# Performance work log

Measured on AMD Instinct MI355X. Metric: run time of the kernel, lower is better.

The kernel has to match this reference:

```python
import jax, jax.numpy as jnp
from jax import lax
import numpy as np

EPS = 1e-08
BETA_VAL = 0.9
B_VAL = 1.0
SIGMA_VAL = 10.0

@jax.custom_vjp
def spike_fn(mthr, sigma):
    # Heaviside forward; SuperSpike surrogate gradient in backward
    return (mthr > 0).astype(mthr.dtype)

def _spike_fwd(mthr, sigma):
    return (mthr > 0).astype(mthr.dtype), (mthr, sigma)

def _spike_bwd(res, g):
    mthr, sigma = res
    grad = g / (sigma * jnp.abs(mthr) + 1.0) ** 2
    return grad, jnp.zeros_like(sigma)

spike_fn.defvjp(_spike_fwd, _spike_bwd)


def setup_inputs() -> dict:
    key = jax.random.key(0)
    kx, kw, kv = jax.random.split(key, 3)
    B, T, I, O = 128, 100, 1024, 1024
    x = jax.random.normal(kx, (B, T, I), dtype=jnp.float32)
    w = (jax.random.normal(kw, (I, O), dtype=jnp.float32)
         * np.float32(np.sqrt(1.0 / I)))  # mean 0, std w_init_std*sqrt(1/I)
    v = (jax.random.normal(kv, (O, O), dtype=jnp.float32)
         * np.float32(np.sqrt(1.0 / O)))
    beta = jnp.full((1,), BETA_VAL, dtype=jnp.float32)   # one_per_layer
    b = jnp.full((O,), B_VAL, dtype=jnp.float32)
    sigma = jnp.full((O,), SIGMA_VAL, dtype=jnp.float32)  # surrogate_sigma_mode='all'
    return {"x": x, "w": w, "v": v, "beta": beta, "b": b, "sigma": sigma}


def reference(x, w, v, beta, b, sigma):
    B, T, I = x.shape
    O = w.shape[1]
    h = jnp.einsum('bti,io->bto', x, w)            # [B,T,O]
    d = jnp.einsum('ai,ao->io', w, w)              # lateral term w^T w, [O,O]
    norm = (w ** 2).sum(0)                         # [O]
    inv_norm = 1.0 / (norm + EPS)

    mem0 = jnp.zeros((B, O), dtype=x.dtype)
    spk0 = jnp.zeros((B, O), dtype=x.dtype)

    def step(carry, h_t):
        mem, spk = carry
        rst = spk @ d                              # lateral reset [B,O]
        inp = h_t + spk @ v                        # recurrent input
        # Leaky neuron, soft reset
        mem = (mem - rst) * beta + inp * (1.0 - beta)
        mthr = mem * inv_norm - b
        spk = spike_fn(mthr, sigma)
        return (mem, spk), spk

    h_t_first = jnp.swapaxes(h, 0, 1)              # [T,B,O]
    _, spk_seq = lax.scan(step, (mem0, spk0), h_t_first)
    spk_rec = jnp.swapaxes(spk_seq, 0, 1)          # [B,T,O]

    loss = 0.5 * (spk_rec ** 2).mean()             # Regularization 'squared'
    spk_spread_loss = spk_rec.sum(axis=(0, 2)).max() / (B * O)  # 'max'
    return spk_rec, loss, spk_spread_loss
```

## Files before the change

### kernel.cpp

```cpp
#include <hip/hip_runtime.h>
#include <cstdint>
#include <cstddef>

#define I_DIM 1024
#define O_DIM 1024
#define B_DIM 128
#define T_DIM 100
#define PANEL 32768
#define QSTep 512

typedef __attribute__((ext_vector_type(8))) __bf16 bf16x8;
typedef __attribute__((ext_vector_type(16))) float f32x16;

__device__ __forceinline__ void wg_barrier_lgkm() {
  __asm__ volatile("" ::: "memory");
  __builtin_amdgcn_s_waitcnt(0xC07F);
  __builtin_amdgcn_s_barrier();
  __asm__ volatile("" ::: "memory");
}

__device__ __forceinline__ unsigned short bf16rn(float x) {
  unsigned u = __float_as_uint(x);
  unsigned r = u + 0x7FFFu + ((u >> 16) & 1u);
  return (unsigned short)(r >> 16);
}
__device__ __forceinline__ void split2(float x, unsigned short& h,
                                       unsigned short& l) {
  h = bf16rn(x);
  float hf = __uint_as_float(((unsigned)h) << 16);
  l = bf16rn(x - hf);
}

__global__ __launch_bounds__(256) void prep_kernel(
    const float* __restrict__ w, const float* __restrict__ x,
    unsigned short* __restrict__ wTth, unsigned short* __restrict__ wTtl,
    unsigned short* __restrict__ xth, unsigned short* __restrict__ xtl,
    double* __restrict__ normpart) {
  __shared__ float tile[64][65];
  __shared__ double red[4][64];
  const int id = blockIdx.x;
  const int tid = threadIdx.x;
  if (id < 256) {
    const int a0 = (id >> 4) * 64, o0 = (id & 15) * 64;
    const int tr = tid >> 4, tc4 = (tid & 15) * 4;
#pragma unroll
    for (int rr = 0; rr < 64; rr += 16) {
      float4 v = *(const float4*)&w[(size_t)(a0 + tr + rr) * O_DIM + o0 + tc4];
      tile[tr + rr][tc4 + 0] = v.x;
      tile[tr + rr][tc4 + 1] = v.y;
      tile[tr + rr][tc4 + 2] = v.z;
      tile[tr + rr][tc4 + 3] = v.w;
    }
    __syncthreads();
    {
      const int ol = tid & 63, seg = tid >> 6;
      double s = 0.0;
#pragma unroll
      for (int i = 0; i < 16; ++i) {
        double v = (double)tile[seg * 16 + i][ol];
        s += v * v;
      }
      red[seg][ol] = s;
    }
    const int q = (a0 >> 4) + (tc4 >> 4);
    const int kh = (tc4 >> 3) & 1;
    const int inner = tc4 & 7;
#pragma unroll
    for (int rr = 0; rr < 64; rr += 16) {
      int o = o0 + tr + rr;
      unsigned short hh[4], ll[4];
#pragma unroll
      for (int j = 0; j < 4; ++j) split2(tile[tc4 + j][tr + rr], hh[j], ll[j]);
      int l = (o & 31) + 32 * kh;
      size_t base = ((size_t)(o >> 5) * PANEL) + (size_t)q * QSTep +
                    (size_t)l * 8 + inner;
      *(ushort4*)&wTth[base] = make_ushort4(hh[0], hh[1], hh[2], hh[3]);
      *(ushort4*)&wTtl[base] = make_ushort4(ll[0], ll[1], ll[2], ll[3]);
    }
    __syncthreads();
    if (tid < 64)
      normpart[(size_t)(a0 >> 6) * O_DIM + o0 + tid] =
          red[0][tid] + red[1][tid] + red[2][tid] + red[3][tid];
  } else {
    const int p = id - 256;
    const int wq = tid >> 6, lane = tid & 63;
    const int row = lane & 31, kh = lane >> 5;
    const float* src = x + (size_t)(p * 32 + row) * I_DIM + kh * 8;
#pragma unroll 4
    for (int i = 0; i < 16; ++i) {
      const int q = i * 4 + wq;
      const float* s = src + q * 16;
      float4 v0 = *(const float4*)(s);
      float4 v1 = *(const float4*)(s + 4);
      unsigned short h[8], l[8];
      split2(v0.x, h[0], l[0]);
      split2(v0.y, h[1], l[1]);
      split2(v0.z, h[2], l[2]);
      split2(v0.w, h[3], l[3]);
      split2(v1.x, h[4], l[4]);
      split2(v1.y, h[5], l[5]);
      split2(v1.z, h[6], l[6]);
      split2(v1.w, h[7], l[7]);
      size_t base = ((size_t)p * PANEL) + (size_t)q * QSTep + (size_t)lane * 8;
      *(ushort4*)&xth[base] = make_ushort4(h[0], h[1], h[2], h[3]);
      *(ushort4*)&xth[base + 4] = make_ushort4(h[4], h[5], h[6], h[7]);
      *(ushort4*)&xtl[base] = make_ushort4(l[0], l[1], l[2], l[3]);
      *(ushort4*)&xtl[base + 4] = make_ushort4(l[4], l[5], l[6], l[7]);
    }
  }
}

__global__ __launch_bounds__(256) void gemm_fused(
    const unsigned short* __restrict__ xth,
    const unsigned short* __restrict__ xtl,
    const unsigned short* __restrict__ wTth,
    const unsigned short* __restrict__ wTtl, const float* __restrict__ v,
    const float* __restrict__ beta_p, float* __restrict__ h,
    float* __restrict__ M) {
  const int tid = threadIdx.x;
  const int wv = tid >> 6, lane = tid & 63;
  const int lm = lane & 31, lkh = lane >> 5;
  if (blockIdx.y < 100) {
    const int row0 = blockIdx.y * 128, col0 = blockIdx.x * 64;
    const int wm = wv >> 1, wn = wv & 1;
    f32x16 acc[2];
#pragma unroll
    for (int a = 0; a < 2; ++a)
#pragma unroll
      for (int e = 0; e < 16; ++e) acc[a][e] = 0.f;
    const unsigned short *pah[2], *pal[2], *pbh, *pbl;
#pragma unroll
    for (int mt = 0; mt < 2; ++mt) {
      size_t offA =
          ((size_t)((row0 >> 5) + wm * 2 + mt) * PANEL) + (size_t)lane * 8;
      pah[mt] = xth + offA;
      pal[mt] = xtl + offA;
    }
    {
      size_t offB = ((size_t)((col0 >> 5) + wn) * PANEL) + (size_t)lane * 8;
      pbh = wTth + offB;
      pbl = wTtl + offB;
    }
    bf16x8 fah[2][2], fal[2][2], fbh[2], fbl[2];
#pragma unroll
    for (int mt = 0; mt < 2; ++mt) {
      fah[0][mt] = *(const bf16x8*)(pah[mt]);
      fal[0][mt] = *(const bf16x8*)(pal[mt]);
    }
    fbh[0] = *(const bf16x8*)(pbh);
    fbl[0] = *(const bf16x8*)(pbl);
#pragma unroll 2
    for (int q = 0; q < 64; ++q) {
      const int cb = q & 1;
      if (q < 63) {
        size_t d = (size_t)(q + 1) * QSTep;
#pragma unroll
        for (int mt = 0; mt < 2; ++mt) {
          fah[cb ^ 1][mt] = *(const bf16x8*)(pah[mt] + d);
          fal[cb ^ 1][mt] = *(const bf16x8*)(pal[mt] + d);
        }
        fbh[cb ^ 1] = *(const bf16x8*)(pbh + d);
        fbl[cb ^ 1] = *(const bf16x8*)(pbl + d);
      }
#pragma unroll
      for (int mt = 0; mt < 2; ++mt)
        acc[mt] = __builtin_amdgcn_mfma_f32_32x32x16_bf16(fah[cb][mt], fbh[cb],
                                                          acc[mt], 0, 0, 0);
#pragma unroll
      for (int mt = 0; mt < 2; ++mt)
        acc[mt] = __builtin_amdgcn_mfma_f32_32x32x16_bf16(fah[cb][mt], fbl[cb],
                                                          acc[mt], 0, 0, 0);
#pragma unroll
      for (int mt = 0; mt < 2; ++mt)
        acc[mt] = __builtin_amdgcn_mfma_f32_32x32x16_bf16(fal[cb][mt], fbh[cb],
                                                          acc[mt], 0, 0, 0);
    }
    const int col = col0 + wn * 32 + lm;
#pragma unroll
    for (int mt = 0; mt < 2; ++mt)
#pragma unroll
      for (int r = 0; r < 16; ++r) {
        int row = row0 + wm * 64 + mt * 32 + (r & 3) + 8 * (r >> 2) + 4 * lkh;
        h[(size_t)row * O_DIM + col] = acc[mt][r];
      }
  } else {
    const int i0 = (blockIdx.y - 100) * 64, o0 = blockIdx.x * 64;
    const int wm = wv >> 1, wn = wv & 1;
    f32x16 acc;
#pragma unroll
    for (int e = 0; e < 16; ++e) acc[e] = 0.f;
    const size_t offA = ((size_t)((i0 >> 5) + wm) * PANEL) + (size_t)lane * 8;
    const size_t offB = ((size_t)((o0 >> 5) + wn) * PANEL) + (size_t)lane * 8;
    bf16x8 ah[2], al[2], bh[2], bl[2];
    ah[0] = *(const bf16x8*)(wTth + offA);
    al[0] = *(const bf16x8*)(wTtl + offA);
    bh[0] = *(const bf16x8*)(wTth + offB);
    bl[0] = *(const bf16x8*)(wTtl + offB);
#pragma unroll 2
    for (int q = 0; q < 64; ++q) {
      const int cb = q & 1;
      if (q < 63) {
        size_t d = (size_t)(q + 1) * QSTep;
        ah[cb ^ 1] = *(const bf16x8*)(wTth + offA + d);
        al[cb ^ 1] = *(const bf16x8*)(wTtl + offA + d);
        bh[cb ^ 1] = *(const bf16x8*)(wTth + offB + d);
        bl[cb ^ 1] = *(const bf16x8*)(wTtl + offB + d);
      }
      acc =
          __builtin_amdgcn_mfma_f32_32x32x16_bf16(ah[cb], bh[cb], acc, 0, 0, 0);
      acc =
          __builtin_amdgcn_mfma_f32_32x32x16_bf16(ah[cb], bl[cb], acc, 0, 0, 0);
      acc =
          __builtin_amdgcn_mfma_f32_32x32x16_bf16(al[cb], bh[cb], acc, 0, 0, 0);
    }
    const float beta = beta_p[0];
    const float ombeta = 1.0f - beta;
    const int col = o0 + wn * 32 + lm;
#pragma unroll
    for (int r = 0; r < 16; ++r) {
      int row = i0 + wm * 32 + (r & 3) + 8 * (r >> 2) + 4 * lkh;
      M[(size_t)row * O_DIM + col] =
          ombeta * v[(size_t)row * O_DIM + col] - beta * acc[r];
    }
  }
}

__global__ __launch_bounds__(256) void scan_kernel(
    const float* __restrict__ h, const float* __restrict__ M,
    const double* __restrict__ normpart, const float* __restrict__ bvec,
    const float* __restrict__ beta_p, float* __restrict__ out,
    int* __restrict__ wgcnt) {
  __shared__ unsigned short wlist[2][4][256];
  __shared__ int wcnt[2][4];
  const int b = blockIdx.x, tid = threadIdx.x;
  const int wv = tid >> 6;
  const double beta = (double)beta_p[0];
  const double ombeta = 1.0 - beta;
  double mem[4] = {0.0, 0.0, 0.0, 0.0};
  double inv[4], bth[4];
  int o[4];
#pragma unroll
  for (int j = 0; j < 4; ++j) {
    o[j] = tid + j * 256;
    double s = 0.0;
#pragma unroll
    for (int g = 0; g < 16; ++g) s += normpart[(size_t)g * O_DIM + o[j]];
    inv[j] = 1.0 / (s + 1e-8);
    bth[j] = (double)bvec[o[j]];
  }
  if (tid < 8) wcnt[tid >> 2][tid & 3] = 0;
  __syncthreads();
  const float* hb = h + (size_t)b * T_DIM * O_DIM;
  float* ob = out + (size_t)b * T_DIM * O_DIM;
  float hv0[4], hv1[4];
#pragma unroll
  for (int j = 0; j < 4; ++j) {
    hv0[j] = hb[o[j]];
    hv1[j] = hb[O_DIM + o[j]];
  }
  for (int t = 0; t < T_DIM; ++t) {
    const int p = t & 1, np = p ^ 1;
    float hv2[4] = {0.f, 0.f, 0.f, 0.f};
    if (t + 2 < T_DIM) {
#pragma unroll
      for (int j = 0; j < 4; ++j) hv2[j] = hb[(size_t)(t + 2) * O_DIM + o[j]];
    }
    double lat[4] = {0.0, 0.0, 0.0, 0.0};
    const int ks = wcnt[p][0] + wcnt[p][1] + wcnt[p][2] + wcnt[p][3];
    if (ks) {
#pragma unroll
      for (int w = 0; w < 4; ++w) {
        const int kw = wcnt[p][w];
        for (int n = 0; n < kw; ++n) {
          const int i = wlist[p][w][n];
          const float* Mrow = M + (size_t)i * O_DIM;
#pragma unroll
          for (int j = 0; j < 4; ++j) lat[j] += (double)Mrow[o[j]];
        }
      }
    }
    unsigned cur = 0;
#pragma unroll
    for (int j = 0; j < 4; ++j) {
      mem[j] = mem[j] * beta + (double)hv0[j] * ombeta + lat[j];
      double mthr = mem[j] * inv[j] - bth[j];
      bool s = mthr > 0.0;
      ob[(size_t)t * O_DIM + o[j]] = s ? 1.0f : 0.0f;
      unsigned long long mask = __ballot(s);
      if (s) {
        unsigned below = __builtin_amdgcn_mbcnt_lo((unsigned)mask, 0);
        below = __builtin_amdgcn_mbcnt_hi((unsigned)(mask >> 32), below);
        wlist[np][wv][cur + below] = (unsigned short)o[j];
      }
      cur += (unsigned)__popcll(mask);
      hv0[j] = hv1[j];
      hv1[j] = hv2[j];
    }
    if ((tid & 63) == 0) wcnt[np][wv] = (int)cur;
    wg_barrier_lgkm();
    if (tid == 0)
      wgcnt[b * T_DIM + t] =
          wcnt[np][0] + wcnt[np][1] + wcnt[np][2] + wcnt[np][3];
  }
}

__global__ void finalize_kernel(const int* __restrict__ wgcnt,
                                float* __restrict__ out) {
  __shared__ int sums[128];
  const int t = threadIdx.x;
  int s = 0;
  if (t < T_DIM) {
    for (int b = 0; b < B_DIM; ++b) s += wgcnt[b * T_DIM + t];
  }
  sums[t] = s;
  __syncthreads();
  if (t == 0) {
    long long total = 0;
    int mx = 0;
    for (int i = 0; i < T_DIM; ++i) {
      total += sums[i];
      if (sums[i] > mx) mx = sums[i];
    }
    const double N = (double)B_DIM * T_DIM * O_DIM;
    out[(size_t)B_DIM * T_DIM * O_DIM] = (float)(0.5 * (double)total / N);
    out[(size_t)B_DIM * T_DIM * O_DIM + 1] =
        (float)((double)mx / (double)(B_DIM * O_DIM));
  }
}

extern "C" void kernel_launch(void* const* d_in, const int* in_sizes, int n_in,
                              void* d_out, int out_size, void* d_ws,
                              size_t ws_size, hipStream_t stream) {
  const float* x = (const float*)d_in[0];
  const float* w = (const float*)d_in[1];
  const float* v = (const float*)d_in[2];
  const float* beta = (const float*)d_in[3];
  const float* b = (const float*)d_in[4];
  float* out = (float*)d_out;

  char* ws = (char*)d_ws;
  const size_t OFF_M = 0;
  const size_t OFF_H = 4194304;
  const size_t OFF_WTH = 56623104;
  const size_t OFF_WTL = 58720256;
  const size_t OFF_NP = 60817408;
  const size_t OFF_XTH = 60948992;
  const size_t OFF_XTL = 87163392;
  float* M = (float*)(ws + OFF_M);
  float* h = (float*)(ws + OFF_H);
  unsigned short* wTth = (unsigned short*)(ws + OFF_WTH);
  unsigned short* wTtl = (unsigned short*)(ws + OFF_WTL);
  double* normpart = (double*)(ws + OFF_NP);
  unsigned short* xth = (unsigned short*)(ws + OFF_XTH);
  unsigned short* xtl = (unsigned short*)(ws + OFF_XTL);
  int* wgcnt = (int*)(ws + OFF_XTH);

  hipLaunchKernelGGL(prep_kernel, dim3(656), dim3(256), 0, stream, w, x, wTth,
                     wTtl, xth, xtl, normpart);
  hipLaunchKernelGGL(gemm_fused, dim3(16, 116), dim3(256), 0, stream, xth, xtl,
                     wTth, wTtl, v, beta, h, M);
  hipLaunchKernelGGL(scan_kernel, dim3(128), dim3(256), 0, stream, h, M,
                     normpart, b, beta, out, wgcnt);
  hipLaunchKernelGGL(finalize_kernel, dim3(1), dim3(128), 0, stream, wgcnt,
                     out);
}
```

Baseline: 306.5 us.

## Split x prep across more blocks, deepen GEMM prefetch, vectorize scan, fuse finalize

Splits each x panel conversion into four blocks so prep launches 1856 blocks instead of 656, giving more parallelism. The GEMM now prefetches two K-steps per iteration and sets launch bounds to three blocks per CU. The scan kernel gives each thread four contiguous outputs so it can use float4 loads of h and M and float4 stores of spikes. The separate finalize kernel is removed: the last scan block to finish, found through an atomic counter, computes the two losses, which saves one launch but adds a memset and a fence.

```diff
diff --git a/kernel.cpp b/kernel.cpp
--- a/kernel.cpp
+++ b/kernel.cpp
@@ -82,12 +82,12 @@
       normpart[(size_t)(a0 >> 6) * O_DIM + o0 + tid] =
           red[0][tid] + red[1][tid] + red[2][tid] + red[3][tid];
   } else {
-    const int p = id - 256;
+    const int p = (id - 256) >> 2, sub = (id - 256) & 3;
     const int wq = tid >> 6, lane = tid & 63;
     const int row = lane & 31, kh = lane >> 5;
     const float* src = x + (size_t)(p * 32 + row) * I_DIM + kh * 8;
-#pragma unroll 4
-    for (int i = 0; i < 16; ++i) {
+#pragma unroll
+    for (int i = sub * 4; i < sub * 4 + 4; ++i) {
       const int q = i * 4 + wq;
       const float* s = src + q * 16;
       float4 v0 = *(const float4*)(s);
@@ -110,7 +110,7 @@
   }
 }
 
-__global__ __launch_bounds__(256) void gemm_fused(
+__global__ __launch_bounds__(256, 3) void gemm_fused(
     const unsigned short* __restrict__ xth,
     const unsigned short* __restrict__ xtl,
     const unsigned short* __restrict__ wTth,
@@ -141,39 +141,50 @@
       pbh = wTth + offB;
       pbl = wTtl + offB;
     }
-    bf16x8 fah[2][2], fal[2][2], fbh[2], fbl[2];
-#pragma unroll
-    for (int mt = 0; mt < 2; ++mt) {
-      fah[0][mt] = *(const bf16x8*)(pah[mt]);
-      fal[0][mt] = *(const bf16x8*)(pal[mt]);
-    }
-    fbh[0] = *(const bf16x8*)(pbh);
-    fbl[0] = *(const bf16x8*)(pbl);
+    bf16x8 fah[2][2][2], fal[2][2][2], fbh[2][2], fbl[2][2];
+#pragma unroll
+    for (int qq = 0; qq < 2; ++qq) {
+      size_t d = (size_t)qq * QSTep;
+#pragma unroll
+      for (int mt = 0; mt < 2; ++mt) {
+        fah[0][qq][mt] = *(const bf16x8*)(pah[mt] + d);
+        fal[0][qq][mt] = *(const bf16x8*)(pal[mt] + d);
+      }
+      fbh[0][qq] = *(const bf16x8*)(pbh + d);
+      fbl[0][qq] = *(const bf16x8*)(pbl + d);
+    }
 #pragma unroll 2
-    for (int q = 0; q < 64; ++q) {
-      const int cb = q & 1;
-      if (q < 63) {
-        size_t d = (size_t)(q + 1) * QSTep;
-#pragma unroll
-        for (int mt = 0; mt < 2; ++mt) {
-          fah[cb ^ 1][mt] = *(const bf16x8*)(pah[mt] + d);
-          fal[cb ^ 1][mt] = *(const bf16x8*)(pal[mt] + d);
+    for (int qp = 0; qp < 32; ++qp) {
+      const int cb = qp & 1;
+      if (qp < 31) {
+        size_t dp = (size_t)(qp + 1) * (2 * QSTep);
+#pragma unroll
+        for (int qq = 0; qq < 2; ++qq) {
+          size_t d = dp + (size_t)qq * QSTep;
+#pragma unroll
+          for (int mt = 0; mt < 2; ++mt) {
+            fah[cb ^ 1][qq][mt] = *(const bf16x8*)(pah[mt] + d);
+            fal[cb ^ 1][qq][mt] = *(const bf16x8*)(pal[mt] + d);
+          }
+          fbh[cb ^ 1][qq] = *(const bf16x8*)(pbh + d);
+          fbl[cb ^ 1][qq] = *(const bf16x8*)(pbl + d);
         }
-        fbh[cb ^ 1] = *(const bf16x8*)(pbh + d);
-        fbl[cb ^ 1] = *(const bf16x8*)(pbl + d);
-      }
-#pragma unroll
-      for (int mt = 0; mt < 2; ++mt)
-        acc[mt] = __builtin_amdgcn_mfma_f32_32x32x16_bf16(fah[cb][mt], fbh[cb],
-                                                          acc[mt], 0, 0, 0);
-#pragma unroll
-      for (int mt = 0; mt < 2; ++mt)
-        acc[mt] = __builtin_amdgcn_mfma_f32_32x32x16_bf16(fah[cb][mt], fbl[cb],
-                                                          acc[mt], 0, 0, 0);
-#pragma unroll
-      for (int mt = 0; mt < 2; ++mt)
-        acc[mt] = __builtin_amdgcn_mfma_f32_32x32x16_bf16(fal[cb][mt], fbh[cb],
-                                                          acc[mt], 0, 0, 0);
+      }
+#pragma unroll
+      for (int qq = 0; qq < 2; ++qq) {
+#pragma unroll
+        for (int mt = 0; mt < 2; ++mt)
+          acc[mt] = __builtin_amdgcn_mfma_f32_32x32x16_bf16(
+              fah[cb][qq][mt], fbh[cb][qq], acc[mt], 0, 0, 0);
+#pragma unroll
+        for (int mt = 0; mt < 2; ++mt)
+          acc[mt] = __builtin_amdgcn_mfma_f32_32x32x16_bf16(
+              fah[cb][qq][mt], fbl[cb][qq], acc[mt], 0, 0, 0);
+#pragma unroll
+        for (int mt = 0; mt < 2; ++mt)
+          acc[mt] = __builtin_amdgcn_mfma_f32_32x32x16_bf16(
+              fal[cb][qq][mt], fbh[cb][qq], acc[mt], 0, 0, 0);
+      }
     }
     const int col = col0 + wn * 32 + lm;
 #pragma unroll
@@ -229,42 +240,36 @@
     const float* __restrict__ h, const float* __restrict__ M,
     const double* __restrict__ normpart, const float* __restrict__ bvec,
     const float* __restrict__ beta_p, float* __restrict__ out,
-    int* __restrict__ wgcnt) {
+    int* __restrict__ wgcnt, int* __restrict__ done) {
   __shared__ unsigned short wlist[2][4][256];
   __shared__ int wcnt[2][4];
+  __shared__ int reds[128];
+  __shared__ int lastflag;
   const int b = blockIdx.x, tid = threadIdx.x;
   const int wv = tid >> 6;
+  const int ob4 = tid * 4;
   const double beta = (double)beta_p[0];
   const double ombeta = 1.0 - beta;
   double mem[4] = {0.0, 0.0, 0.0, 0.0};
   double inv[4], bth[4];
-  int o[4];
 #pragma unroll
   for (int j = 0; j < 4; ++j) {
-    o[j] = tid + j * 256;
     double s = 0.0;
 #pragma unroll
-    for (int g = 0; g < 16; ++g) s += normpart[(size_t)g * O_DIM + o[j]];
+    for (int g = 0; g < 16; ++g) s += normpart[(size_t)g * O_DIM + ob4 + j];
     inv[j] = 1.0 / (s + 1e-8);
-    bth[j] = (double)bvec[o[j]];
+    bth[j] = (double)bvec[ob4 + j];
   }
   if (tid < 8) wcnt[tid >> 2][tid & 3] = 0;
   __syncthreads();
   const float* hb = h + (size_t)b * T_DIM * O_DIM;
-  float* ob = out + (size_t)b * T_DIM * O_DIM;
-  float hv0[4], hv1[4];
-#pragma unroll
-  for (int j = 0; j < 4; ++j) {
-    hv0[j] = hb[o[j]];
-    hv1[j] = hb[O_DIM + o[j]];
-  }
+  float* obp = out + (size_t)b * T_DIM * O_DIM;
+  float4 hv0 = *(const float4*)&hb[ob4];
+  float4 hv1 = *(const float4*)&hb[O_DIM + ob4];
   for (int t = 0; t < T_DIM; ++t) {
     const int p = t & 1, np = p ^ 1;
-    float hv2[4] = {0.f, 0.f, 0.f, 0.f};
-    if (t + 2 < T_DIM) {
-#pragma unroll
-      for (int j = 0; j < 4; ++j) hv2[j] = hb[(size_t)(t + 2) * O_DIM + o[j]];
-    }
+    float4 hv2 = make_float4(0.f, 0.f, 0.f, 0.f);
+    if (t + 2 < T_DIM) hv2 = *(const float4*)&hb[(size_t)(t + 2) * O_DIM + ob4];
     double lat[4] = {0.0, 0.0, 0.0, 0.0};
     const int ks = wcnt[p][0] + wcnt[p][1] + wcnt[p][2] + wcnt[p][3];
     if (ks) {
@@ -273,58 +278,67 @@
         const int kw = wcnt[p][w];
         for (int n = 0; n < kw; ++n) {
           const int i = wlist[p][w][n];
-          const float* Mrow = M + (size_t)i * O_DIM;
-#pragma unroll
-          for (int j = 0; j < 4; ++j) lat[j] += (double)Mrow[o[j]];
+          float4 m = *(const float4*)&M[(size_t)i * O_DIM + ob4];
+          lat[0] += (double)m.x;
+          lat[1] += (double)m.y;
+          lat[2] += (double)m.z;
+          lat[3] += (double)m.w;
         }
       }
     }
+    const float hvv[4] = {hv0.x, hv0.y, hv0.z, hv0.w};
+    float os[4];
     unsigned cur = 0;
 #pragma unroll
     for (int j = 0; j < 4; ++j) {
-      mem[j] = mem[j] * beta + (double)hv0[j] * ombeta + lat[j];
+      mem[j] = mem[j] * beta + (double)hvv[j] * ombeta + lat[j];
       double mthr = mem[j] * inv[j] - bth[j];
       bool s = mthr > 0.0;
-      ob[(size_t)t * O_DIM + o[j]] = s ? 1.0f : 0.0f;
+      os[j] = s ? 1.0f : 0.0f;
       unsigned long long mask = __ballot(s);
       if (s) {
         unsigned below = __builtin_amdgcn_mbcnt_lo((unsigned)mask, 0);
         below = __builtin_amdgcn_mbcnt_hi((unsigned)(mask >> 32), below);
-        wlist[np][wv][cur + below] = (unsigned short)o[j];
+        wlist[np][wv][cur + below] = (unsigned short)(ob4 + j);
       }
       cur += (unsigned)__popcll(mask);
-      hv0[j] = hv1[j];
-      hv1[j] = hv2[j];
-    }
+    }
+    *(float4*)&obp[(size_t)t * O_DIM + ob4] =
+        make_float4(os[0], os[1], os[2], os[3]);
+    hv0 = hv1;
+    hv1 = hv2;
     if ((tid & 63) == 0) wcnt[np][wv] = (int)cur;
     wg_barrier_lgkm();
     if (tid == 0)
       wgcnt[b * T_DIM + t] =
           wcnt[np][0] + wcnt[np][1] + wcnt[np][2] + wcnt[np][3];
   }
-}
-
-__global__ void finalize_kernel(const int* __restrict__ wgcnt,
-                                float* __restrict__ out) {
-  __shared__ int sums[128];
-  const int t = threadIdx.x;
-  int s = 0;
-  if (t < T_DIM) {
-    for (int b = 0; b < B_DIM; ++b) s += wgcnt[b * T_DIM + t];
-  }
-  sums[t] = s;
+  __threadfence();
+  if (tid == 0) {
+    int old = atomicAdd(done, 1);
+    lastflag = (old == B_DIM - 1) ? 1 : 0;
+  }
   __syncthreads();
-  if (t == 0) {
-    long long total = 0;
-    int mx = 0;
-    for (int i = 0; i < T_DIM; ++i) {
-      total += sums[i];
-      if (sums[i] > mx) mx = sums[i];
-    }
-    const double N = (double)B_DIM * T_DIM * O_DIM;
-    out[(size_t)B_DIM * T_DIM * O_DIM] = (float)(0.5 * (double)total / N);
-    out[(size_t)B_DIM * T_DIM * O_DIM + 1] =
-        (float)((double)mx / (double)(B_DIM * O_DIM));
+  if (lastflag) {
+    __threadfence();
+    int s = 0;
+    if (tid < T_DIM) {
+      for (int bb = 0; bb < B_DIM; ++bb) s += wgcnt[bb * T_DIM + tid];
+    }
+    if (tid < 128) reds[tid] = (tid < T_DIM) ? s : 0;
+    __syncthreads();
+    if (tid == 0) {
+      long long total = 0;
+      int mx = 0;
+      for (int i = 0; i < T_DIM; ++i) {
+        total += reds[i];
+        if (reds[i] > mx) mx = reds[i];
+      }
+      const double N = (double)B_DIM * T_DIM * O_DIM;
+      out[(size_t)B_DIM * T_DIM * O_DIM] = (float)(0.5 * (double)total / N);
+      out[(size_t)B_DIM * T_DIM * O_DIM + 1] =
+          (float)((double)mx / (double)(B_DIM * O_DIM));
+    }
   }
 }
 
@@ -344,6 +358,7 @@
   const size_t OFF_WTH = 56623104;
   const size_t OFF_WTL = 58720256;
   const size_t OFF_NP = 60817408;
+  const size_t OFF_DONE = 60948480;
   const size_t OFF_XTH = 60948992;
   const size_t OFF_XTL = 87163392;
   float* M = (float*)(ws + OFF_M);
@@ -351,16 +366,16 @@
   unsigned short* wTth = (unsigned short*)(ws + OFF_WTH);
   unsigned short* wTtl = (unsigned short*)(ws + OFF_WTL);
   double* normpart = (double*)(ws + OFF_NP);
+  int* done = (int*)(ws + OFF_DONE);
   unsigned short* xth = (unsigned short*)(ws + OFF_XTH);
   unsigned short* xtl = (unsigned short*)(ws + OFF_XTL);
   int* wgcnt = (int*)(ws + OFF_XTH);
 
-  hipLaunchKernelGGL(prep_kernel, dim3(656), dim3(256), 0, stream, w, x, wTth,
+  hipMemsetAsync(done, 0, 512, stream);
+  hipLaunchKernelGGL(prep_kernel, dim3(1856), dim3(256), 0, stream, w, x, wTth,
                      wTtl, xth, xtl, normpart);
   hipLaunchKernelGGL(gemm_fused, dim3(16, 116), dim3(256), 0, stream, xth, xtl,
                      wTth, wTtl, v, beta, h, M);
   hipLaunchKernelGGL(scan_kernel, dim3(128), dim3(256), 0, stream, h, M,
-                     normpart, b, beta, out, wgcnt);
-  hipLaunchKernelGGL(finalize_kernel, dim3(1), dim3(128), 0, stream, wgcnt,
-                     out);
-}
+                     normpart, b, beta, out, wgcnt, done);
+}
```

Result: slower. 321.5 us (+4.9%).
